# Performance work log

Hardware: AMD Instinct MI355X
Metric: run time of the kernel (lower is better)

The kernel has to match this reference:

```python
import jax, jax.numpy as jnp
import numpy as np

# The original module sorts x by key x*rho, then solves per-row the separable QP
#   min sum_i (rho_i * (a_i - sorted_x_i))^2  s.t.  a_i + c_i >= 0
# whose closed-form solution is a_i = max(sorted_x_i, -c_i) (rho_i^2 > 0 cancels),
# then un-sorts back to the original order. We implement exactly that math.

B = 4096
P = 8192

def setup_inputs() -> dict:
    key = jax.random.key(0)
    kx, kr, kc = jax.random.split(key, 3)
    x = jax.random.normal(kx, (B, P), dtype=jnp.float32)
    rho = jax.random.uniform(kr, (B, P), dtype=jnp.float32) + 0.1  # positive weights
    c = jax.random.uniform(kc, (P,), dtype=jnp.float32)
    return {"x": x, "rho": rho, "c": c}

def reference(x, rho, c):
    # sort each row by key x*rho
    sorted_args = jnp.argsort(x * rho, axis=-1)                      # [B, P] int
    sorted_x = jnp.take_along_axis(x, sorted_args, axis=-1)          # [B, P]
    # closed-form box-constrained QP solution: clamp to lower bound -c (c is in sorted-position order)
    answer = jnp.maximum(sorted_x, -c)                               # broadcast c over batch
    # unsort back to original order
    re_sort = jnp.argsort(sorted_args, axis=-1)
    return jnp.take_along_axis(answer, re_sort, axis=-1)
```

## Files before the change

kernel.cpp:

```cpp
#include <hip/hip_runtime.h>


constexpr int P_LEN  = 8192;
constexpr int BDIM   = 1024;
constexpr int EPT    = P_LEN / BDIM;
constexpr int NW     = BDIM / 64;
constexpr int CWORDS = P_LEN / 2;
constexpr int WIN    = 8;

__device__ __forceinline__ unsigned fkey(float f) {
    unsigned u = __float_as_uint(f);
    return (u & 0x80000000u) ? ~u : (u | 0x80000000u);
}

__device__ __forceinline__ unsigned pk_word(unsigned v) { return v & (CWORDS - 1u); }
__device__ __forceinline__ unsigned pk_inc(unsigned v)  { return (v & (unsigned)CWORDS) ? 0x10000u : 1u; }
__device__ __forceinline__ unsigned pk_get(unsigned w, unsigned v) { return (w >> ((v >> 12) << 4)) & 0xFFFFu; }
__device__ __forceinline__ unsigned pk_us(unsigned v)   { return ((v & (CWORDS - 1u)) << 1) | (v >> 12); }

__device__ __forceinline__ void scan_packed(unsigned* cnt, unsigned* wt,
                                            int t, int lane, int wid)
{
    uint4 cw = ((const uint4*)cnt)[t];
    const unsigned p1 = cw.x, p2 = cw.x + cw.y, p3 = cw.x + cw.y + cw.z;
    const unsigned s  = p3 + cw.w;
    unsigned incl = s;
#pragma unroll
    for (int d = 1; d < 64; d <<= 1) {
        unsigned v = __shfl_up(incl, d, 64);
        if (lane >= d) incl += v;
    }
    if (lane == 63) wt[wid] = incl;
    __syncthreads();
    if (t < 64) {
        unsigned v = (lane < NW) ? wt[lane] : 0u;
        const unsigned orig = v;
#pragma unroll
        for (int d = 1; d < NW; d <<= 1) {
            unsigned u = __shfl_up(v, d, 64);
            if (lane >= d) v += u;
        }
        if (lane < NW)     wt[lane] = v - orig;
        if (lane == NW - 1) wt[NW]  = v;
    }
    __syncthreads();
    const unsigned base = wt[wid] + (incl - s);
    const unsigned totL = wt[NW] & 0xFFFFu;
    const unsigned q0 = base, q1 = base + p1, q2 = base + p2, q3 = base + p3;
    uint4 out;
    out.x = (q0 & 0xFFFFu) | ((totL + (q0 >> 16)) << 16);
    out.y = (q1 & 0xFFFFu) | ((totL + (q1 >> 16)) << 16);
    out.z = (q2 & 0xFFFFu) | ((totL + (q2 >> 16)) << 16);
    out.w = (q3 & 0xFFFFu) | ((totL + (q3 >> 16)) << 16);
    ((uint4*)cnt)[t] = out;
    __syncthreads();
}

__global__ __launch_bounds__(BDIM, 8)
void qp_rank_kernel(const float* __restrict__ x,
                    const float* __restrict__ rho,
                    const float* __restrict__ c,
                    float* __restrict__ out)
{
    __shared__ unsigned cnt[CWORDS];
    __shared__ unsigned mem[P_LEN + WIN];
    __shared__ unsigned wt[NW + 1];

    const int row  = blockIdx.x;
    const int t    = threadIdx.x;
    const int j0   = t * EPT;
    const int lane = t & 63;
    const int wid  = t >> 6;

    const float* __restrict__ xr   = x   + (size_t)row * P_LEN;
    const float* __restrict__ rr   = rho + (size_t)row * P_LEN;
    float*       __restrict__ outr = out + (size_t)row * P_LEN;
    const unsigned short* usview = (const unsigned short*)cnt;

    const uint4 z4 = make_uint4(0u, 0u, 0u, 0u);
    ((uint4*)cnt)[t] = z4;
    __syncthreads();

    float4 xa = ((const float4*)(xr + j0))[0];
    float4 xb = ((const float4*)(xr + j0))[1];
    float4 ra = ((const float4*)(rr + j0))[0];
    float4 rb = ((const float4*)(rr + j0))[1];
    float xs[EPT] = {xa.x, xa.y, xa.z, xa.w, xb.x, xb.y, xb.z, xb.w};
    float rs[EPT] = {ra.x, ra.y, ra.z, ra.w, rb.x, rb.y, rb.z, rb.w};
    unsigned key[EPT];
#pragma unroll
    for (int k = 0; k < EPT; ++k) {
        key[k] = fkey(xs[k] * rs[k]);
        const unsigned b = key[k] >> 19;
        atomicAdd(&cnt[pk_word(b)], pk_inc(b));
    }
    __syncthreads();

    scan_packed(cnt, wt, t, lane, wid);

    unsigned bin2[EPT];
#pragma unroll
    for (int k = 0; k < EPT; ++k) {
        const unsigned b   = key[k] >> 19;
        const unsigned s_b = usview[pk_us(b)];
        const unsigned e_b = (b == (unsigned)(P_LEN - 1)) ? (unsigned)P_LEN
                                                          : usview[pk_us(b + 1)];
        const unsigned sz  = e_b - s_b;
        const unsigned r   = (key[k] >> 6) & 0x1FFFu;
        bin2[k] = s_b + ((sz * r) >> 13);
    }
    __syncthreads();

    ((uint4*)cnt)[t] = z4;
    __syncthreads();
#pragma unroll
    for (int k = 0; k < EPT; ++k)
        atomicAdd(&cnt[pk_word(bin2[k])], pk_inc(bin2[k]));
    __syncthreads();

    scan_packed(cnt, wt, t, lane, wid);

    unsigned mine[EPT];
#pragma unroll
    for (int k = 0; k < EPT; ++k) {
        mine[k] = (key[k] << 13) | (unsigned)(j0 + k);
        const unsigned b2 = bin2[k];
        const unsigned old = atomicAdd(&cnt[pk_word(b2)], pk_inc(b2));
        mem[pk_get(old, b2)] = mine[k];
    }
    __syncthreads();

    unsigned rnk[EPT];
#pragma unroll
    for (int k = 0; k < EPT; ++k) {
        const unsigned b2 = bin2[k];
        const unsigned lo = (b2 == 0u) ? 0u : usview[pk_us(b2 - 1)];
        const unsigned hi = usview[pk_us(b2)];
        const unsigned m  = mine[k];
        const unsigned* mp = mem + lo;
        unsigned w[WIN];
#pragma unroll
        for (int i = 0; i < WIN; ++i) w[i] = mp[i];
        unsigned r = lo;
#pragma unroll
        for (int i = 0; i < WIN; ++i)
            r += ((lo + (unsigned)i < hi) && (w[i] < m)) ? 1u : 0u;
        unsigned q = lo + WIN;
#pragma unroll 1
        while (q < hi) { r += (mem[q] < m) ? 1u : 0u; ++q; }
        rnk[k] = r;
    }

    float res[EPT];
#pragma unroll
    for (int k = 0; k < EPT; ++k) res[k] = fmaxf(xs[k], -c[rnk[k]]);
    ((float4*)(outr + j0))[0] = make_float4(res[0], res[1], res[2], res[3]);
    ((float4*)(outr + j0))[1] = make_float4(res[4], res[5], res[6], res[7]);
}

extern "C" void kernel_launch(void* const* d_in, const int* in_sizes, int n_in,
                              void* d_out, int out_size, void* d_ws, size_t ws_size,
                              hipStream_t stream) {
    const float* x   = (const float*)d_in[0];
    const float* rho = (const float*)d_in[1];
    const float* c   = (const float*)d_in[2];
    float* out = (float*)d_out;
    const int rows = in_sizes[0] / P_LEN;
    qp_rank_kernel<<<rows, BDIM, 0, stream>>>(x, rho, c, out);
}
```

Baseline: 354.2 us.

## Halve block size to 512 threads with 16 elements per thread and redundant wave-total scan

Reduces the block to 512 threads so each thread handles 16 elements and scans 8 packed counter words. The cross-wave scan is replaced by every thread summing the 8 wave totals itself, which removes one barrier. x is re-read from global in the final pass instead of being held in registers, and the window size is cut to 4. The aim is to lower register pressure and synchronisation cost. In exchange each thread does more serial work, and fewer waves per block may reduce latency hiding.

```diff
diff --git a/kernel.cpp b/kernel.cpp
--- a/kernel.cpp
+++ b/kernel.cpp
@@ -2,11 +2,12 @@
 
 
 constexpr int P_LEN  = 8192;
-constexpr int BDIM   = 1024;
+constexpr int BDIM   = 512;
 constexpr int EPT    = P_LEN / BDIM;
 constexpr int NW     = BDIM / 64;
 constexpr int CWORDS = P_LEN / 2;
-constexpr int WIN    = 8;
+constexpr int WPT    = CWORDS / BDIM;
+constexpr int WIN    = 4;
 
 __device__ __forceinline__ unsigned fkey(float f) {
     unsigned u = __float_as_uint(f);
@@ -21,9 +22,14 @@
 __device__ __forceinline__ void scan_packed(unsigned* cnt, unsigned* wt,
                                             int t, int lane, int wid)
 {
-    uint4 cw = ((const uint4*)cnt)[t];
-    const unsigned p1 = cw.x, p2 = cw.x + cw.y, p3 = cw.x + cw.y + cw.z;
-    const unsigned s  = p3 + cw.w;
+    uint4 ca = ((const uint4*)cnt)[t * 2];
+    uint4 cb = ((const uint4*)cnt)[t * 2 + 1];
+    unsigned p[WPT] = {ca.x, ca.y, ca.z, ca.w, cb.x, cb.y, cb.z, cb.w};
+    unsigned pre[WPT];
+    unsigned s = 0;
+#pragma unroll
+    for (int i = 0; i < WPT; ++i) { pre[i] = s; s += p[i]; }
+
     unsigned incl = s;
 #pragma unroll
     for (int d = 1; d < 64; d <<= 1) {
@@ -32,31 +38,27 @@
     }
     if (lane == 63) wt[wid] = incl;
     __syncthreads();
-    if (t < 64) {
-        unsigned v = (lane < NW) ? wt[lane] : 0u;
-        const unsigned orig = v;
+    unsigned waveBase = 0, tot = 0;
 #pragma unroll
-        for (int d = 1; d < NW; d <<= 1) {
-            unsigned u = __shfl_up(v, d, 64);
-            if (lane >= d) v += u;
-        }
-        if (lane < NW)     wt[lane] = v - orig;
-        if (lane == NW - 1) wt[NW]  = v;
+    for (int w = 0; w < NW; ++w) {
+        const unsigned v = wt[w];
+        waveBase += (w < wid) ? v : 0u;
+        tot += v;
     }
-    __syncthreads();
-    const unsigned base = wt[wid] + (incl - s);
-    const unsigned totL = wt[NW] & 0xFFFFu;
-    const unsigned q0 = base, q1 = base + p1, q2 = base + p2, q3 = base + p3;
-    uint4 out;
-    out.x = (q0 & 0xFFFFu) | ((totL + (q0 >> 16)) << 16);
-    out.y = (q1 & 0xFFFFu) | ((totL + (q1 >> 16)) << 16);
-    out.z = (q2 & 0xFFFFu) | ((totL + (q2 >> 16)) << 16);
-    out.w = (q3 & 0xFFFFu) | ((totL + (q3 >> 16)) << 16);
-    ((uint4*)cnt)[t] = out;
+    const unsigned base = waveBase + (incl - s);
+    const unsigned totL = tot & 0xFFFFu;
+    unsigned q[WPT];
+#pragma unroll
+    for (int i = 0; i < WPT; ++i) {
+        const unsigned qi = base + pre[i];
+        q[i] = (qi & 0xFFFFu) | ((totL + (qi >> 16)) << 16);
+    }
+    ((uint4*)cnt)[t * 2]     = make_uint4(q[0], q[1], q[2], q[3]);
+    ((uint4*)cnt)[t * 2 + 1] = make_uint4(q[4], q[5], q[6], q[7]);
     __syncthreads();
 }
 
-__global__ __launch_bounds__(BDIM, 8)
+__global__ __launch_bounds__(BDIM, 6)
 void qp_rank_kernel(const float* __restrict__ x,
                     const float* __restrict__ rho,
                     const float* __restrict__ c,
@@ -64,7 +66,7 @@
 {
     __shared__ unsigned cnt[CWORDS];
     __shared__ unsigned mem[P_LEN + WIN];
-    __shared__ unsigned wt[NW + 1];
+    __shared__ unsigned wt[NW];
 
     const int row  = blockIdx.x;
     const int t    = threadIdx.x;
@@ -78,19 +80,28 @@
     const unsigned short* usview = (const unsigned short*)cnt;
 
     const uint4 z4 = make_uint4(0u, 0u, 0u, 0u);
-    ((uint4*)cnt)[t] = z4;
+    ((uint4*)cnt)[t * 2]     = z4;
+    ((uint4*)cnt)[t * 2 + 1] = z4;
     __syncthreads();
 
-    float4 xa = ((const float4*)(xr + j0))[0];
-    float4 xb = ((const float4*)(xr + j0))[1];
-    float4 ra = ((const float4*)(rr + j0))[0];
-    float4 rb = ((const float4*)(rr + j0))[1];
-    float xs[EPT] = {xa.x, xa.y, xa.z, xa.w, xb.x, xb.y, xb.z, xb.w};
-    float rs[EPT] = {ra.x, ra.y, ra.z, ra.w, rb.x, rb.y, rb.z, rb.w};
     unsigned key[EPT];
+    {
+        float4 xv[EPT / 4], rv[EPT / 4];
+#pragma unroll
+        for (int v = 0; v < EPT / 4; ++v) {
+            xv[v] = ((const float4*)(xr + j0))[v];
+            rv[v] = ((const float4*)(rr + j0))[v];
+        }
+#pragma unroll
+        for (int v = 0; v < EPT / 4; ++v) {
+            key[v * 4 + 0] = fkey(xv[v].x * rv[v].x);
+            key[v * 4 + 1] = fkey(xv[v].y * rv[v].y);
+            key[v * 4 + 2] = fkey(xv[v].z * rv[v].z);
+            key[v * 4 + 3] = fkey(xv[v].w * rv[v].w);
+        }
+    }
 #pragma unroll
     for (int k = 0; k < EPT; ++k) {
-        key[k] = fkey(xs[k] * rs[k]);
         const unsigned b = key[k] >> 19;
         atomicAdd(&cnt[pk_word(b)], pk_inc(b));
     }
@@ -111,7 +122,8 @@
     }
     __syncthreads();
 
-    ((uint4*)cnt)[t] = z4;
+    ((uint4*)cnt)[t * 2]     = z4;
+    ((uint4*)cnt)[t * 2 + 1] = z4;
     __syncthreads();
 #pragma unroll
     for (int k = 0; k < EPT; ++k)
@@ -120,42 +132,45 @@
 
     scan_packed(cnt, wt, t, lane, wid);
 
-    unsigned mine[EPT];
 #pragma unroll
     for (int k = 0; k < EPT; ++k) {
-        mine[k] = (key[k] << 13) | (unsigned)(j0 + k);
-        const unsigned b2 = bin2[k];
+        const unsigned b2  = bin2[k];
         const unsigned old = atomicAdd(&cnt[pk_word(b2)], pk_inc(b2));
-        mem[pk_get(old, b2)] = mine[k];
+        mem[pk_get(old, b2)] = (key[k] << 13) | (unsigned)(j0 + k);
     }
     __syncthreads();
 
-    unsigned rnk[EPT];
 #pragma unroll
-    for (int k = 0; k < EPT; ++k) {
-        const unsigned b2 = bin2[k];
-        const unsigned lo = (b2 == 0u) ? 0u : usview[pk_us(b2 - 1)];
-        const unsigned hi = usview[pk_us(b2)];
-        const unsigned m  = mine[k];
-        const unsigned* mp = mem + lo;
-        unsigned w[WIN];
+    for (int g = 0; g < EPT / 4; ++g) {
+        const float4 xg = ((const float4*)(xr + j0))[g];
+        unsigned rk[4];
 #pragma unroll
-        for (int i = 0; i < WIN; ++i) w[i] = mp[i];
-        unsigned r = lo;
+        for (int kk = 0; kk < 4; ++kk) {
+            const int k = g * 4 + kk;
+            const unsigned b2 = bin2[k];
+            const unsigned lo = (b2 == 0u) ? 0u : usview[pk_us(b2 - 1)];
+            const unsigned hi = usview[pk_us(b2)];
+            const unsigned m  = (key[k] << 13) | (unsigned)(j0 + k);
+            const unsigned* mp = mem + lo;
+            unsigned w[WIN];
 #pragma unroll
-        for (int i = 0; i < WIN; ++i)
-            r += ((lo + (unsigned)i < hi) && (w[i] < m)) ? 1u : 0u;
-        unsigned q = lo + WIN;
+            for (int i = 0; i < WIN; ++i) w[i] = mp[i];
+            unsigned r = lo;
+#pragma unroll
+            for (int i = 0; i < WIN; ++i)
+                r += ((lo + (unsigned)i < hi) && (w[i] < m)) ? 1u : 0u;
+            unsigned q = lo + WIN;
 #pragma unroll 1
-        while (q < hi) { r += (mem[q] < m) ? 1u : 0u; ++q; }
-        rnk[k] = r;
+            while (q < hi) { r += (mem[q] < m) ? 1u : 0u; ++q; }
+            rk[kk] = r;
+        }
+        float4 res;
+        res.x = fmaxf(xg.x, -c[rk[0]]);
+        res.y = fmaxf(xg.y, -c[rk[1]]);
+        res.z = fmaxf(xg.z, -c[rk[2]]);
+        res.w = fmaxf(xg.w, -c[rk[3]]);
+        ((float4*)(outr + j0))[g] = res;
     }
-
-    float res[EPT];
-#pragma unroll
-    for (int k = 0; k < EPT; ++k) res[k] = fmaxf(xs[k], -c[rnk[k]]);
-    ((float4*)(outr + j0))[0] = make_float4(res[0], res[1], res[2], res[3]);
-    ((float4*)(outr + j0))[1] = make_float4(res[4], res[5], res[6], res[7]);
 }
 
 extern "C" void kernel_launch(void* const* d_in, const int* in_sizes, int n_in,
```

New measurement: 418.2 us. 18.1% more time.
